# Optimization experiments

Measured on AMD Instinct MI355X. Metric: run time of the kernel, lower is better.

## Reference

```python
import jax, jax.numpy as jnp
import numpy as np

DEPTH = 6
N_LEAF = 2 ** DEPTH          # 64
GATE_COUNT = N_LEAF - 1      # 63
IN_F = 512
OUT_F = 512
BATCH = 1024


def setup_inputs() -> dict:
    key = jax.random.key(0)
    k1, k2, k3 = jax.random.split(key, 3)
    x = jax.random.normal(k1, (BATCH, IN_F), dtype=jnp.float32)
    gw = jax.random.normal(k2, (IN_F, GATE_COUNT), dtype=jnp.float32)
    gb = jnp.zeros((GATE_COUNT,), dtype=jnp.float32)
    pw = jax.random.normal(k3, (OUT_F, IN_F, N_LEAF), dtype=jnp.float32)
    pb = jnp.zeros((OUT_F, N_LEAF), dtype=jnp.float32)
    return {"x": x, "gw": gw, "gb": gb, "pw": pw, "pb": pb}


def _leaf_probs(x, gw, gb, depth):
    # gatings: sigmoid(x @ gw + gb), shape [B, gate_count]
    g = jax.nn.sigmoid(x @ gw + gb)
    B = x.shape[0]
    dens = jnp.ones((B, 1), dtype=x.dtype)  # root density
    offset = 0
    for d in range(depth):
        n = 2 ** d
        gp = g[:, offset:offset + n]                    # parent gatings [B, n]
        # left child multiplies by g, right child by (1 - g), interleaved
        pair = jnp.stack([gp, 1.0 - gp], axis=-1).reshape(B, 2 * n)
        dens = jnp.repeat(dens, 2, axis=1) * pair        # [B, 2n]
        offset += n
    return dens  # [B, n_leaf]


def reference(x, gw, gb, pw, pb):
    leaf = _leaf_probs(x, gw, gb, DEPTH)                 # [B, L]
    # per-leaf linear projections, then mix with leaf probabilities
    y = jnp.einsum('bi,oil->bol', x, pw)                 # [B, O, L]
    out = jnp.einsum('bol,bl->bo', y, leaf) + leaf @ pb.T
    return out
```

## Files before the change

### kernel.cpp

```cpp
#include <hip/hip_runtime.h>
#include <hip/hip_bf16.h>

#define TDEPTH 6
#define NLEAF 64
#define NGATE 63
#define INF 512
#define OUTF 512
#define BATCH 1024

#define BM 128
#define BN 64
#define SPLITK 16
#define THREADS 256
#define KCH 513
#define XN 32

typedef __attribute__((ext_vector_type(4)))  float f32x4;
typedef __attribute__((ext_vector_type(16))) float f32x16;
typedef __attribute__((ext_vector_type(8)))  __bf16 bf16x8;

__global__ __launch_bounds__(256) void leaf_kernel(
    const float* __restrict__ x, const float* __restrict__ gw,
    const float* __restrict__ gb, float* __restrict__ leaf) {
  const int wid = threadIdx.x >> 6, lane = threadIdx.x & 63;
  const int b = blockIdx.x * 4 + wid;
  __shared__ float g[4][NLEAF];
  if (lane < NGATE) {
    const float* xr = x + (size_t)b * INF;
    float a0 = 0.f, a1 = 0.f, a2 = 0.f, a3 = 0.f;
    #pragma unroll 4
    for (int i = 0; i < INF; i += 4) {
      a0 += xr[i + 0] * gw[(i + 0) * NGATE + lane];
      a1 += xr[i + 1] * gw[(i + 1) * NGATE + lane];
      a2 += xr[i + 2] * gw[(i + 2) * NGATE + lane];
      a3 += xr[i + 3] * gw[(i + 3) * NGATE + lane];
    }
    float t = (a0 + a1) + (a2 + a3) + gb[lane];
    g[wid][lane] = 1.0f / (1.0f + __expf(-t));
  }
  __syncthreads();
  float p = 1.0f;
  #pragma unroll
  for (int d = 0; d < TDEPTH; d++) {
    int prefix = lane >> (TDEPTH - 1 - d);
    int node = (1 << d) - 1 + (prefix >> 1);
    float gv = g[wid][node];
    p *= (prefix & 1) ? (1.0f - gv) : gv;
  }
  leaf[(size_t)b * NLEAF + lane] = p;
}

__device__ __forceinline__ void gload_lds16(const void* g, void* l) {
  __builtin_amdgcn_global_load_lds(
      (const __attribute__((address_space(1))) void*)g,
      (__attribute__((address_space(3))) void*)l, 16, 0, 0);
}

__global__ __launch_bounds__(THREADS, 4) void gemm_kernel(
    const float* __restrict__ x, const float* __restrict__ pw,
    const float* __restrict__ pb, const float* __restrict__ leaf,
    float* __restrict__ partial) {
  __shared__ __align__(16) unsigned char Bsm[2][BN * 256];
  __shared__ __align__(16) __bf16 xsm[XN * BM];

  const int tid = threadIdx.x, lane = tid & 63, w = tid >> 6;
  const int lo = lane & 31, half = lane >> 5;

  const int L = (blockIdx.x & 7) * 128 + (blockIdx.x >> 3);
  const int mb = L & 7;
  const int rest = L >> 3;
  const int nb = rest & 7, s = rest >> 3;
  const int m0 = mb * BM, n0 = nb * BN;
  const int cs = XN * s;
  const int total = XN + ((s == SPLITK - 1) ? 1 : 0);

  f32x4 lf[4][2];
  {
    const float* lr = leaf + (size_t)(m0 + w * 32 + lo) * NLEAF + half * 8;
    #pragma unroll
    for (int t4 = 0; t4 < 4; t4++) {
      lf[t4][0] = *(const f32x4*)(lr + t4 * 16);
      lf[t4][1] = *(const f32x4*)(lr + t4 * 16 + 4);
    }
  }

  {
    const int row = tid >> 1, h = tid & 1;
    const float* src = x + (size_t)(m0 + row) * INF + cs + h * 16;
    #pragma unroll
    for (int c4 = 0; c4 < 4; c4++) {
      f32x4 v = *(const f32x4*)(src + c4 * 4);
      #pragma unroll
      for (int j = 0; j < 4; j++)
        xsm[(h * 16 + c4 * 4 + j) * BM + row] = (__bf16)v[j];
    }
  }

  const int lq = lane >> 4;
  const unsigned cg = (unsigned)(lane & 15);
  const unsigned gsw = (cg ^ ((unsigned)(4 * w + lq) & 15)) * 16;
  unsigned pwoff[4], pboff[4];
  #pragma unroll
  for (int j = 0; j < 4; j++) {
    int r = j * 16 + 4 * w + lq;
    pwoff[j] = (unsigned)(n0 + r) * (unsigned)(INF * NLEAF * 4) + gsw;
    pboff[j] = (unsigned)(n0 + r) * (unsigned)(NLEAF * 4) + gsw;
  }
  const char* pwc = (const char*)pw;
  const char* pbc = (const char*)pb;

  auto stage = [&](char* dstb, int t) {
    const int i = cs + t;
    if (i < INF) {
      const char* srcb = pwc + (size_t)i * 256;
      #pragma unroll
      for (int j = 0; j < 4; j++)
        gload_lds16(srcb + pwoff[j], dstb + (j * 16 + 4 * w) * 256);
    } else {
      #pragma unroll
      for (int j = 0; j < 4; j++)
        gload_lds16(pbc + pboff[j], dstb + (j * 16 + 4 * w) * 256);
    }
  };

  f32x16 acc0 = (f32x16)(0.f), acc1 = (f32x16)(0.f);
  const unsigned swz = (unsigned)(lo & 15) << 4;

  auto do_step = [&](const char* bufc, int t) {
    const float xv = (t < XN) ? (float)xsm[t * BM + w * 32 + lo] : 1.0f;
    #pragma unroll
    for (int t4 = 0; t4 < 4; t4++) {
      const unsigned kb = (unsigned)(t4 * 64 + half * 32);
      f32x4 b0a = *(const f32x4*)(bufc + lo * 256 + ((kb) ^ swz));
      f32x4 b0b = *(const f32x4*)(bufc + lo * 256 + ((kb + 16) ^ swz));
      f32x4 b1a = *(const f32x4*)(bufc + (32 + lo) * 256 + ((kb) ^ swz));
      f32x4 b1b = *(const f32x4*)(bufc + (32 + lo) * 256 + ((kb + 16) ^ swz));
      bf16x8 bf0, bf1;
      bf0[0] = (__bf16)b0a[0]; bf0[1] = (__bf16)b0a[1];
      bf0[2] = (__bf16)b0a[2]; bf0[3] = (__bf16)b0a[3];
      bf0[4] = (__bf16)b0b[0]; bf0[5] = (__bf16)b0b[1];
      bf0[6] = (__bf16)b0b[2]; bf0[7] = (__bf16)b0b[3];
      bf1[0] = (__bf16)b1a[0]; bf1[1] = (__bf16)b1a[1];
      bf1[2] = (__bf16)b1a[2]; bf1[3] = (__bf16)b1a[3];
      bf1[4] = (__bf16)b1b[0]; bf1[5] = (__bf16)b1b[1];
      bf1[6] = (__bf16)b1b[2]; bf1[7] = (__bf16)b1b[3];

      f32x4 pa = lf[t4][0] * xv, pbv = lf[t4][1] * xv;
      bf16x8 a;
      a[0] = (__bf16)pa[0]; a[1] = (__bf16)pa[1];
      a[2] = (__bf16)pa[2]; a[3] = (__bf16)pa[3];
      a[4] = (__bf16)pbv[0]; a[5] = (__bf16)pbv[1];
      a[6] = (__bf16)pbv[2]; a[7] = (__bf16)pbv[3];

      acc0 = __builtin_amdgcn_mfma_f32_32x32x16_bf16(a, bf0, acc0, 0, 0, 0);
      acc1 = __builtin_amdgcn_mfma_f32_32x32x16_bf16(a, bf1, acc1, 0, 0, 0);
    }
  };

  char* bA = (char*)&Bsm[0][0];
  char* bB = (char*)&Bsm[1][0];

  stage(bA, 0);
  __builtin_amdgcn_sched_barrier(0);
  asm volatile("s_waitcnt vmcnt(0) lgkmcnt(0)" ::: "memory");
  __builtin_amdgcn_s_barrier();
  __builtin_amdgcn_sched_barrier(0);

  for (int t = 0; t < total; ++t) {
    if (t + 1 < total) stage(bB, t + 1);
    do_step(bA, t);
    __builtin_amdgcn_sched_barrier(0);
    asm volatile("s_waitcnt vmcnt(0)" ::: "memory");
    __builtin_amdgcn_s_barrier();
    __builtin_amdgcn_sched_barrier(0);
    char* tmp = bA; bA = bB; bB = tmp;
  }

  float* dst = partial + ((size_t)s * BATCH + m0 + w * 32) * OUTF + n0;
  #pragma unroll
  for (int e = 0; e < 16; e++) {
    int row = (e & 3) + 8 * (e >> 2) + 4 * half;
    dst[(size_t)row * OUTF + lo] = acc0[e];
    dst[(size_t)row * OUTF + 32 + lo] = acc1[e];
  }
}

__global__ __launch_bounds__(256) void reduce_kernel(
    const float* __restrict__ partial, float* __restrict__ out) {
  size_t e = ((size_t)blockIdx.x * 256 + threadIdx.x) * 4;
  f32x4 sum = (f32x4){0.f, 0.f, 0.f, 0.f};
  #pragma unroll
  for (int s = 0; s < SPLITK; s++)
    sum += *(const f32x4*)(partial + (size_t)s * BATCH * OUTF + e);
  *(f32x4*)(out + e) = sum;
}

extern "C" void kernel_launch(void* const* d_in, const int* in_sizes, int n_in,
                              void* d_out, int out_size, void* d_ws, size_t ws_size,
                              hipStream_t stream) {
  const float* x  = (const float*)d_in[0];
  const float* gw = (const float*)d_in[1];
  const float* gb = (const float*)d_in[2];
  const float* pw = (const float*)d_in[3];
  const float* pb = (const float*)d_in[4];
  float* out = (float*)d_out;

  float* leaf    = (float*)d_ws;
  float* partial = (float*)((char*)d_ws + (1 << 20));

  leaf_kernel<<<BATCH / 4, 256, 0, stream>>>(x, gw, gb, leaf);
  gemm_kernel<<<8 * 8 * SPLITK, THREADS, 0, stream>>>(x, pw, pb, leaf, partial);
  reduce_kernel<<<(BATCH * OUTF) / (256 * 4), 256, 0, stream>>>(partial, out);
}
```

Baseline: 77.43 us.

## Pre-convert projection weights to swizzled bf16 and triple-buffer the GEMM B stages

A prep kernel now converts pw and pb from fp32 into a pre-swizzled bf16 copy in workspace, and the leaf-probability computation is merged into the same launch. The GEMM streams half as many bytes per stage and no longer converts B fragments in registers. Its pipeline moves from double to triple buffering, waiting with vmcnt(2). The cost is an extra full read of pw (about 64MB) plus a 32MB write on every call, which may outweigh the bytes the GEMM saves.

```diff
diff --git a/kernel.cpp b/kernel.cpp
--- a/kernel.cpp
+++ b/kernel.cpp
@@ -12,42 +12,69 @@
 #define BN 64
 #define SPLITK 16
 #define THREADS 256
-#define KCH 513
 #define XN 32
+#define PWG (512 * 512 * 8)
+#define PBG (512 * 8)
 
 typedef __attribute__((ext_vector_type(4)))  float f32x4;
 typedef __attribute__((ext_vector_type(16))) float f32x16;
 typedef __attribute__((ext_vector_type(8)))  __bf16 bf16x8;
 
-__global__ __launch_bounds__(256) void leaf_kernel(
+__global__ __launch_bounds__(256) void prep_kernel(
     const float* __restrict__ x, const float* __restrict__ gw,
-    const float* __restrict__ gb, float* __restrict__ leaf) {
-  const int wid = threadIdx.x >> 6, lane = threadIdx.x & 63;
-  const int b = blockIdx.x * 4 + wid;
-  __shared__ float g[4][NLEAF];
-  if (lane < NGATE) {
-    const float* xr = x + (size_t)b * INF;
-    float a0 = 0.f, a1 = 0.f, a2 = 0.f, a3 = 0.f;
-    #pragma unroll 4
-    for (int i = 0; i < INF; i += 4) {
-      a0 += xr[i + 0] * gw[(i + 0) * NGATE + lane];
-      a1 += xr[i + 1] * gw[(i + 1) * NGATE + lane];
-      a2 += xr[i + 2] * gw[(i + 2) * NGATE + lane];
-      a3 += xr[i + 3] * gw[(i + 3) * NGATE + lane];
-    }
-    float t = (a0 + a1) + (a2 + a3) + gb[lane];
-    g[wid][lane] = 1.0f / (1.0f + __expf(-t));
-  }
-  __syncthreads();
-  float p = 1.0f;
-  #pragma unroll
-  for (int d = 0; d < TDEPTH; d++) {
-    int prefix = lane >> (TDEPTH - 1 - d);
-    int node = (1 << d) - 1 + (prefix >> 1);
-    float gv = g[wid][node];
-    p *= (prefix & 1) ? (1.0f - gv) : gv;
-  }
-  leaf[(size_t)b * NLEAF + lane] = p;
+    const float* __restrict__ gb, const float* __restrict__ pw,
+    const float* __restrict__ pb, float* __restrict__ leaf,
+    __bf16* __restrict__ pwb, __bf16* __restrict__ pbb) {
+  const int tid = threadIdx.x;
+  if (blockIdx.x < 256) {
+    const int wid = tid >> 6, lane = tid & 63;
+    const int b = blockIdx.x * 4 + wid;
+    __shared__ float g[4][NLEAF];
+    if (lane < NGATE) {
+      const float* xr = x + (size_t)b * INF;
+      float a0 = 0.f, a1 = 0.f, a2 = 0.f, a3 = 0.f;
+      #pragma unroll 4
+      for (int i = 0; i < INF; i += 4) {
+        a0 += xr[i + 0] * gw[(i + 0) * NGATE + lane];
+        a1 += xr[i + 1] * gw[(i + 1) * NGATE + lane];
+        a2 += xr[i + 2] * gw[(i + 2) * NGATE + lane];
+        a3 += xr[i + 3] * gw[(i + 3) * NGATE + lane];
+      }
+      float t = (a0 + a1) + (a2 + a3) + gb[lane];
+      g[wid][lane] = 1.0f / (1.0f + __expf(-t));
+    }
+    __syncthreads();
+    float p = 1.0f;
+    #pragma unroll
+    for (int d = 0; d < TDEPTH; d++) {
+      int prefix = lane >> (TDEPTH - 1 - d);
+      int node = (1 << d) - 1 + (prefix >> 1);
+      float gv = g[wid][node];
+      p *= (prefix & 1) ? (1.0f - gv) : gv;
+    }
+    leaf[(size_t)b * NLEAF + lane] = p;
+  } else {
+    const unsigned G = (blockIdx.x - 256) * 256 + tid;
+    const float* src;
+    char* dst;
+    if (G < PWG) {
+      unsigned o = G >> 12, rem = G & 4095, i = rem >> 3, gg = rem & 7;
+      src = pw + ((size_t)(o * 512 + i) * 64 + gg * 8);
+      dst = (char*)pwb + ((size_t)(o * 512 + i) * 8 + (gg ^ (o & 7))) * 16;
+    } else {
+      unsigned G2 = G - PWG;
+      unsigned o = G2 >> 3, gg = G2 & 7;
+      src = pb + ((size_t)o * 64 + gg * 8);
+      dst = (char*)pbb + ((size_t)o * 8 + (gg ^ (o & 7))) * 16;
+    }
+    f32x4 a = *(const f32x4*)src, b = *(const f32x4*)(src + 4);
+    bf16x8 wv;
+    wv[0] = (__bf16)a[0]; wv[1] = (__bf16)a[1];
+    wv[2] = (__bf16)a[2]; wv[3] = (__bf16)a[3];
+    wv[4] = (__bf16)b[0]; wv[5] = (__bf16)b[1];
+    wv[6] = (__bf16)b[2]; wv[7] = (__bf16)b[3];
+    *(bf16x8*)dst = wv;
+  }
 }
 
 __device__ __forceinline__ void gload_lds16(const void* g, void* l) {
@@ -57,10 +84,10 @@
 }
 
 __global__ __launch_bounds__(THREADS, 4) void gemm_kernel(
-    const float* __restrict__ x, const float* __restrict__ pw,
-    const float* __restrict__ pb, const float* __restrict__ leaf,
+    const __bf16* __restrict__ pwb, const __bf16* __restrict__ pbb,
+    const float* __restrict__ x, const float* __restrict__ leaf,
     float* __restrict__ partial) {
-  __shared__ __align__(16) unsigned char Bsm[2][BN * 256];
+  __shared__ __align__(16) __bf16 Bsm[3][BN * 64];
   __shared__ __align__(16) __bf16 xsm[XN * BM];
 
   const int tid = threadIdx.x, lane = tid & 63, w = tid >> 6;
@@ -96,62 +123,46 @@
     }
   }
 
-  const int lq = lane >> 4;
-  const unsigned cg = (unsigned)(lane & 15);
-  const unsigned gsw = (cg ^ ((unsigned)(4 * w + lq) & 15)) * 16;
-  unsigned pwoff[4], pboff[4];
+  size_t pwoff[2], pboff[2];
   #pragma unroll
-  for (int j = 0; j < 4; j++) {
-    int r = j * 16 + 4 * w + lq;
-    pwoff[j] = (unsigned)(n0 + r) * (unsigned)(INF * NLEAF * 4) + gsw;
-    pboff[j] = (unsigned)(n0 + r) * (unsigned)(NLEAF * 4) + gsw;
-  }
-  const char* pwc = (const char*)pw;
-  const char* pbc = (const char*)pb;
+  for (int j = 0; j < 2; j++) {
+    int r = j * 32 + w * 8 + (lane >> 3);
+    pwoff[j] = (size_t)(n0 + r) * (512 * 128) + (size_t)(lane & 7) * 16;
+    pboff[j] = (size_t)(n0 + r) * 128 + (size_t)(lane & 7) * 16;
+  }
+  const char* pwc = (const char*)pwb;
+  const char* pbc = (const char*)pbb;
 
   auto stage = [&](char* dstb, int t) {
     const int i = cs + t;
     if (i < INF) {
-      const char* srcb = pwc + (size_t)i * 256;
       #pragma unroll
-      for (int j = 0; j < 4; j++)
-        gload_lds16(srcb + pwoff[j], dstb + (j * 16 + 4 * w) * 256);
+      for (int j = 0; j < 2; j++)
+        gload_lds16(pwc + pwoff[j] + (size_t)i * 128,
+                    dstb + j * 4096 + w * 1024);
     } else {
       #pragma unroll
-      for (int j = 0; j < 4; j++)
-        gload_lds16(pbc + pboff[j], dstb + (j * 16 + 4 * w) * 256);
+      for (int j = 0; j < 2; j++)
+        gload_lds16(pbc + pboff[j], dstb + j * 4096 + w * 1024);
     }
   };
 
   f32x16 acc0 = (f32x16)(0.f), acc1 = (f32x16)(0.f);
-  const unsigned swz = (unsigned)(lo & 15) << 4;
+  const unsigned swz = (unsigned)(lo & 7) << 4;
 
   auto do_step = [&](const char* bufc, int t) {
     const float xv = (t < XN) ? (float)xsm[t * BM + w * 32 + lo] : 1.0f;
     #pragma unroll
     for (int t4 = 0; t4 < 4; t4++) {
-      const unsigned kb = (unsigned)(t4 * 64 + half * 32);
-      f32x4 b0a = *(const f32x4*)(bufc + lo * 256 + ((kb) ^ swz));
-      f32x4 b0b = *(const f32x4*)(bufc + lo * 256 + ((kb + 16) ^ swz));
-      f32x4 b1a = *(const f32x4*)(bufc + (32 + lo) * 256 + ((kb) ^ swz));
-      f32x4 b1b = *(const f32x4*)(bufc + (32 + lo) * 256 + ((kb + 16) ^ swz));
-      bf16x8 bf0, bf1;
-      bf0[0] = (__bf16)b0a[0]; bf0[1] = (__bf16)b0a[1];
-      bf0[2] = (__bf16)b0a[2]; bf0[3] = (__bf16)b0a[3];
-      bf0[4] = (__bf16)b0b[0]; bf0[5] = (__bf16)b0b[1];
-      bf0[6] = (__bf16)b0b[2]; bf0[7] = (__bf16)b0b[3];
-      bf1[0] = (__bf16)b1a[0]; bf1[1] = (__bf16)b1a[1];
-      bf1[2] = (__bf16)b1a[2]; bf1[3] = (__bf16)b1a[3];
-      bf1[4] = (__bf16)b1b[0]; bf1[5] = (__bf16)b1b[1];
-      bf1[6] = (__bf16)b1b[2]; bf1[7] = (__bf16)b1b[3];
-
+      const unsigned kb = ((unsigned)(t4 * 32 + half * 16)) ^ swz;
+      bf16x8 bf0 = *(const bf16x8*)(bufc + lo * 128 + kb);
+      bf16x8 bf1 = *(const bf16x8*)(bufc + (32 + lo) * 128 + kb);
       f32x4 pa = lf[t4][0] * xv, pbv = lf[t4][1] * xv;
       bf16x8 a;
       a[0] = (__bf16)pa[0]; a[1] = (__bf16)pa[1];
       a[2] = (__bf16)pa[2]; a[3] = (__bf16)pa[3];
       a[4] = (__bf16)pbv[0]; a[5] = (__bf16)pbv[1];
       a[6] = (__bf16)pbv[2]; a[7] = (__bf16)pbv[3];
-
       acc0 = __builtin_amdgcn_mfma_f32_32x32x16_bf16(a, bf0, acc0, 0, 0, 0);
       acc1 = __builtin_amdgcn_mfma_f32_32x32x16_bf16(a, bf1, acc1, 0, 0, 0);
     }
@@ -159,22 +170,30 @@
 
   char* bA = (char*)&Bsm[0][0];
   char* bB = (char*)&Bsm[1][0];
+  char* bC = (char*)&Bsm[2][0];
 
   stage(bA, 0);
-  __builtin_amdgcn_sched_barrier(0);
-  asm volatile("s_waitcnt vmcnt(0) lgkmcnt(0)" ::: "memory");
+  stage(bB, 1);
+  __builtin_amdgcn_sched_barrier(0);
+  asm volatile("s_waitcnt vmcnt(2) lgkmcnt(0)" ::: "memory");
   __builtin_amdgcn_s_barrier();
   __builtin_amdgcn_sched_barrier(0);
 
-  for (int t = 0; t < total; ++t) {
-    if (t + 1 < total) stage(bB, t + 1);
+  for (int t = 0; t < total - 2; ++t) {
+    stage(bC, t + 2);
     do_step(bA, t);
     __builtin_amdgcn_sched_barrier(0);
-    asm volatile("s_waitcnt vmcnt(0)" ::: "memory");
+    asm volatile("s_waitcnt vmcnt(2)" ::: "memory");
     __builtin_amdgcn_s_barrier();
     __builtin_amdgcn_sched_barrier(0);
-    char* tmp = bA; bA = bB; bB = tmp;
-  }
+    char* tmp = bA; bA = bB; bB = bC; bC = tmp;
+  }
+  do_step(bA, total - 2);
+  __builtin_amdgcn_sched_barrier(0);
+  asm volatile("s_waitcnt vmcnt(0)" ::: "memory");
+  __builtin_amdgcn_s_barrier();
+  __builtin_amdgcn_sched_barrier(0);
+  do_step(bB, total - 1);
 
   float* dst = partial + ((size_t)s * BATCH + m0 + w * 32) * OUTF + n0;
   #pragma unroll
@@ -205,10 +224,13 @@
   const float* pb = (const float*)d_in[4];
   float* out = (float*)d_out;
 
-  float* leaf    = (float*)d_ws;
-  float* partial = (float*)((char*)d_ws + (1 << 20));
-
-  leaf_kernel<<<BATCH / 4, 256, 0, stream>>>(x, gw, gb, leaf);
-  gemm_kernel<<<8 * 8 * SPLITK, THREADS, 0, stream>>>(x, pw, pb, leaf, partial);
+  float*  leaf    = (float*)d_ws;
+  __bf16* pbb     = (__bf16*)((char*)d_ws + (256 << 10));
+  __bf16* pwb     = (__bf16*)((char*)d_ws + (1 << 20));
+  float*  partial = (float*)((char*)d_ws + (1 << 20) + (32 << 20));
+
+  prep_kernel<<<256 + (PWG + PBG) / 256, 256, 0, stream>>>(
+      x, gw, gb, pw, pb, leaf, pwb, pbb);
+  gemm_kernel<<<8 * 8 * SPLITK, THREADS, 0, stream>>>(pwb, pbb, x, leaf, partial);
   reduce_kernel<<<(BATCH * OUTF) / (256 * 4), 256, 0, stream>>>(partial, out);
 }
```

After: 75.08 us. 3.0% less time.
